# Kernel tuning notes

Measured on AMD Instinct MI355X. Metric: run time of the kernel, lower is better.

The kernel has to match this reference:

```python
import jax, jax.numpy as jnp
import numpy as np

N, E, D, H = 50000, 800000, 128, 128


def _uniform_param(key, shape, fan_in):
    bound = 1.0 / np.sqrt(fan_in)
    return jax.random.uniform(key, shape, jnp.float32, -bound, bound)


def setup_inputs() -> dict:
    key = jax.random.key(0)
    ks = jax.random.split(key, 12)
    x = jax.random.normal(ks[0], (N, D), jnp.float32)
    xedge = jax.random.randint(ks[1], (2, E), 0, N, jnp.int64)
    y = jax.random.randint(ks[2], (N,), 0, 2, jnp.int32).astype(bool)
    return {
        "x": x,
        "xedge": xedge,
        "y": y,
        "pretrain": 0,
        # SAGEConv layer 1 (in=D, out=H): lin_l (with bias) applied to mean aggr, lin_r (no bias) to self
        "W1l": _uniform_param(ks[3], (D, H), D),
        "b1l": _uniform_param(ks[4], (H,), D),
        "W1r": _uniform_param(ks[5], (D, H), D),
        # SAGEConv layer 2 (in=H, out=H)
        "W2l": _uniform_param(ks[6], (H, H), H),
        "b2l": _uniform_param(ks[7], (H,), H),
        "W2r": _uniform_param(ks[8], (H, H), H),
        # Decoder weight [H, H]
        "Wdec": _uniform_param(ks[9], (H, H), H),
    }


def sage_conv(h, src, dst, Wl, bl, Wr, num_nodes):
    # gather neighbor features along edges, mean-aggregate by destination
    msgs = h[src]                                            # [E, d]
    agg = jax.ops.segment_sum(msgs, dst, num_segments=num_nodes)
    cnt = jax.ops.segment_sum(jnp.ones((src.shape[0],), h.dtype), dst,
                              num_segments=num_nodes)
    mean = agg / jnp.maximum(cnt, 1.0)[:, None]              # [N, d]
    return mean @ Wl + bl + h @ Wr                           # [N, out]


def reference(x, xedge, y, pretrain, W1l, b1l, W1r, W2l, b2l, W2r, Wdec):
    src, dst = xedge[0], xedge[1]
    n = x.shape[0]
    # Encoder: SAGE = conv1 -> relu -> (dropout: eval identity) -> conv2
    h = jax.nn.relu(sage_conv(x, src, dst, W1l, b1l, W1r, n))
    emb = sage_conv(h, src, dst, W2l, b2l, W2r, n)           # [N, H]
    # Decoder
    dx = emb @ Wdec                                          # [N, H]
    # BCEWithLogits: pos nodes target 1, neg nodes target 0, mean within each group
    ym = y.astype(dx.dtype)                                  # [N]
    n_pos = jnp.sum(ym)
    n_neg = n - n_pos
    hdim = dx.shape[1]
    sp_pos = jax.nn.softplus(-dx)   # bce(logit, 1)
    sp_neg = jax.nn.softplus(dx)    # bce(logit, 0)
    l2 = jnp.sum(sp_pos * ym[:, None]) / (jnp.maximum(n_pos, 1.0) * hdim)
    l1 = jnp.sum(sp_neg * (1.0 - ym)[:, None]) / (jnp.maximum(n_neg, 1.0) * hdim)
    return (l1 + l2, emb)
```

## Files before the change

kernel.cpp:

```cpp
#include <hip/hip_runtime.h>
#include <hip/hip_bf16.h>

#define NDIM 128
#define SCAN_CHUNK 1024

typedef __attribute__((ext_vector_type(8))) short short8;
typedef __attribute__((ext_vector_type(4))) float f32x4;

__device__ __forceinline__ float bf2f(__hip_bfloat16 v) { return __bfloat162float(v); }

__device__ __forceinline__ float ldf(const void* p, long i, int f32) {
    return f32 ? ((const float*)p)[i] : bf2f(((const __hip_bfloat16*)p)[i]);
}
__device__ __forceinline__ void stf(void* p, long i, int f32, float v) {
    if (f32) ((float*)p)[i] = v;
    else     ((__hip_bfloat16*)p)[i] = __float2bfloat16(v);
}
__device__ __forceinline__ short f2bf(float v) {
    __hip_bfloat16 h = __float2bfloat16(v);
    short s;
    __builtin_memcpy(&s, &h, 2);
    return s;
}
__device__ __forceinline__ float bflo(unsigned u) { u <<= 16; float f; __builtin_memcpy(&f, &u, 4); return f; }
__device__ __forceinline__ float bfhi(unsigned u) { u &= 0xffff0000u; float f; __builtin_memcpy(&f, &u, 4); return f; }
__device__ __forceinline__ unsigned packbf(float a, float b) {
    unsigned la = (unsigned short)f2bf(a);
    unsigned hb = (unsigned short)f2bf(b);
    return (hb << 16) | la;
}
__device__ __forceinline__ int aswz(int m, int k) {
    return m * NDIM + ((((k >> 3) ^ (m & 7)) << 3) | (k & 7));
}
__device__ __forceinline__ int wswz(int m, int p) {
    return m * 64 + ((((p >> 2) ^ (m & 7)) << 2) | (p & 3));
}

__global__ void detect_kernel(const int* __restrict__ xedge32,
                              const unsigned int* __restrict__ yw,
                              const unsigned short* __restrict__ xh,
                              int* __restrict__ flags, int* __restrict__ cnt,
                              float* __restrict__ accum, int* __restrict__ npos, int N) {
    const int gid = blockIdx.x * 256 + threadIdx.x;
    for (int i = gid; i < N; i += gridDim.x * 256) cnt[i] = 0;
    if (gid == 0) { accum[0] = 0.f; accum[1] = 0.f; npos[0] = 0; }
    if (blockIdx.x == 0) {
        __shared__ int se, sy, scount;
        const int t = threadIdx.x;
        if (t == 0) { se = 1; sy = 0; scount = 0; }
        __syncthreads();
        for (int i = t; i < 512; i += 256)
            if (xedge32[2 * i + 1] != 0) se = 0;
        for (int i = t; i < 1024; i += 256)
            if (yw[i] > 1u) sy = 1;
        int c = 0;
        for (int i = t; i < 1024; i += 256) {
            int ex = (xh[2 * i] >> 7) & 0xFF;
            if (ex >= 100 && ex <= 150) c++;
        }
        atomicAdd(&scount, c);
        __syncthreads();
        if (t == 0) { flags[0] = se; flags[1] = sy; flags[2] = (scount < 900) ? 1 : 0; }
    }
}


__global__ void prep_kernel(const void* __restrict__ x,
                            const void* __restrict__ W1l, const void* __restrict__ b1l,
                            const void* __restrict__ W1r, const void* __restrict__ W2l,
                            const void* __restrict__ b2l, const void* __restrict__ W2r,
                            const void* __restrict__ Wd, const int* __restrict__ flags,
                            short* __restrict__ T1l, short* __restrict__ T1r,
                            short* __restrict__ T2l, short* __restrict__ T2r,
                            short* __restrict__ Td, float* __restrict__ b1c,
                            float* __restrict__ b2c, unsigned* __restrict__ xb, int N) {
    const int wf = flags[2];
    const long idx = (long)blockIdx.x * 256 + threadIdx.x;
    if (idx < NDIM * NDIM) {
        int k = (int)(idx >> 7), n = (int)(idx & 127);
        int o = n * NDIM + k;
        T1l[o] = f2bf(ldf(W1l, idx, wf));
        T1r[o] = f2bf(ldf(W1r, idx, wf));
        T2l[o] = f2bf(ldf(W2l, idx, wf));
        T2r[o] = f2bf(ldf(W2r, idx, wf));
        Td [o] = f2bf(ldf(Wd , idx, wf));
        if (idx < NDIM) { b1c[idx] = ldf(b1l, idx, wf); b2c[idx] = ldf(b2l, idx, wf); }
    } else {
        long p = idx - NDIM * NDIM;
        long np = (long)N * 64;
        if (p < np) {
            if (wf) {
                float2 v = ((const float2*)x)[p];
                xb[p] = packbf(v.x, v.y);
            } else {
                xb[p] = ((const unsigned*)x)[p];
            }
        }
    }
}


__global__ void degree_kernel(const int* __restrict__ xedge, int E,
                              const int* __restrict__ flags, int* __restrict__ cnt) {
    int e = blockIdx.x * blockDim.x + threadIdx.x;
    if (e >= E) return;
    int d = flags[0] ? xedge[2 * (E + e)] : xedge[E + e];
    atomicAdd(&cnt[d], 1);
}


__global__ void scan_partial(const int* __restrict__ cnt, int* __restrict__ bsum, int N) {
    __shared__ int red[256];
    const int t = threadIdx.x;
    const long base = (long)blockIdx.x * SCAN_CHUNK + (long)t * 4;
    int s = 0;
#pragma unroll
    for (int i = 0; i < 4; ++i) { long idx = base + i; if (idx < N) s += cnt[idx]; }
    red[t] = s;
    __syncthreads();
    for (int off = 128; off >= 1; off >>= 1) {
        if (t < off) red[t] += red[t + off];
        __syncthreads();
    }
    if (t == 0) bsum[blockIdx.x] = red[0];
}

__global__ void scan_bsums(const int* __restrict__ bsum, int* __restrict__ boff,
                           int B, int* __restrict__ rowptr, int N) {
    __shared__ int part[1024];
    const int t = threadIdx.x;
    int v = (t < B) ? bsum[t] : 0;
    part[t] = v;
    __syncthreads();
    for (int off = 1; off < 1024; off <<= 1) {
        int u = (t >= off) ? part[t - off] : 0;
        __syncthreads();
        part[t] += u;
        __syncthreads();
    }
    if (t < B) boff[t] = part[t] - v;
    if (t == 1023) rowptr[N] = part[1023];
}

__global__ void scan_scatter(int* __restrict__ cnt, const int* __restrict__ boff,
                             int* __restrict__ rowptr, int N) {
    __shared__ int tsum[256];
    const int t = threadIdx.x;
    const long base = (long)blockIdx.x * SCAN_CHUNK + (long)t * 4;
    int loc[4];
    int s = 0;
#pragma unroll
    for (int i = 0; i < 4; ++i) {
        long idx = base + i;
        int c = (idx < N) ? cnt[idx] : 0;
        loc[i] = s;
        s += c;
    }
    tsum[t] = s;
    __syncthreads();
    for (int off = 1; off < 256; off <<= 1) {
        int u = (t >= off) ? tsum[t - off] : 0;
        __syncthreads();
        tsum[t] += u;
        __syncthreads();
    }
    const int texcl = tsum[t] - s;
    const int b0 = boff[blockIdx.x];
#pragma unroll
    for (int i = 0; i < 4; ++i) {
        long idx = base + i;
        if (idx < N) { rowptr[idx] = b0 + texcl + loc[i]; cnt[idx] = 0; }
    }
}

__global__ void fill_kernel(const int* __restrict__ xedge, int E,
                            const int* __restrict__ flags, const int* __restrict__ rowptr,
                            int* __restrict__ cur, int* __restrict__ col) {
    int e = blockIdx.x * blockDim.x + threadIdx.x;
    if (e >= E) return;
    const int e64 = flags[0];
    int s = e64 ? xedge[2 * e] : xedge[e];
    int d = e64 ? xedge[2 * (E + e)] : xedge[E + e];
    int p = rowptr[d] + atomicAdd(&cur[d], 1);
    col[p] = s;
}


template <bool RELU, int OUTMODE>
__global__ __launch_bounds__(256)
void layer_mfma(const unsigned* __restrict__ Xb, const int* __restrict__ rowptr,
                const int* __restrict__ col, const short* __restrict__ WlT,
                const float* __restrict__ biasc, const short* __restrict__ WrT,
                const int* __restrict__ flags, void* __restrict__ outp, int N) {
    __shared__ short Ms[32 * NDIM];
    __shared__ short Ss[32 * NDIM];
    unsigned* Msw = (unsigned*)Ms;
    unsigned* Ssw = (unsigned*)Ss;
    const int t = threadIdx.x;
    const int n0 = blockIdx.x * 32;
    const int wf = flags[2];
    {
        const int g = t >> 6, p = t & 63;
        for (int r = g; r < 32; r += 4) {
            int n = n0 + r;
            float m0 = 0.f, m1 = 0.f;
            unsigned su = 0;
            if (n < N) {
                int b = rowptr[n], e = rowptr[n + 1];
                int i = b;
                for (; i + 8 <= e; i += 8) {
                    unsigned u0 = Xb[(long)col[i    ] * 64 + p];
                    unsigned u1 = Xb[(long)col[i + 1] * 64 + p];
                    unsigned u2 = Xb[(long)col[i + 2] * 64 + p];
                    unsigned u3 = Xb[(long)col[i + 3] * 64 + p];
                    unsigned u4 = Xb[(long)col[i + 4] * 64 + p];
                    unsigned u5 = Xb[(long)col[i + 5] * 64 + p];
                    unsigned u6 = Xb[(long)col[i + 6] * 64 + p];
                    unsigned u7 = Xb[(long)col[i + 7] * 64 + p];
                    m0 += ((bflo(u0) + bflo(u1)) + (bflo(u2) + bflo(u3)))
                        + ((bflo(u4) + bflo(u5)) + (bflo(u6) + bflo(u7)));
                    m1 += ((bfhi(u0) + bfhi(u1)) + (bfhi(u2) + bfhi(u3)))
                        + ((bfhi(u4) + bfhi(u5)) + (bfhi(u6) + bfhi(u7)));
                }
                for (; i < e; ++i) {
                    unsigned u = Xb[(long)col[i] * 64 + p];
                    m0 += bflo(u);
                    m1 += bfhi(u);
                }
                float inv = 1.f / fmaxf((float)(e - b), 1.f);
                m0 *= inv; m1 *= inv;
                su = Xb[(long)n * 64 + p];
            }
            int wi = wswz(r, p);
            Msw[wi] = packbf(m0, m1);
            Ssw[wi] = su;
        }
    }
    __syncthreads();
    const int l = t & 63, w = t >> 6;
    const int quad = l >> 4, l15 = l & 15;
    const int wcol = w * 32;
    f32x4 acc[2][2] = {};
    for (int k0 = 0; k0 < NDIM; k0 += 32) {
        const int kc = k0 + quad * 8;
        short8 ams[2], ass[2], bl[2], br[2];
#pragma unroll
        for (int rt = 0; rt < 2; ++rt) {
            int m = rt * 16 + l15;
            ams[rt] = *(const short8*)&Ms[aswz(m, kc)];
            ass[rt] = *(const short8*)&Ss[aswz(m, kc)];
        }
#pragma unroll
        for (int ct = 0; ct < 2; ++ct) {
            int n = wcol + ct * 16 + l15;
            bl[ct] = *(const short8*)&WlT[n * NDIM + kc];
            br[ct] = *(const short8*)&WrT[n * NDIM + kc];
        }
#pragma unroll
        for (int rt = 0; rt < 2; ++rt)
#pragma unroll
            for (int ct = 0; ct < 2; ++ct) {
                acc[rt][ct] = __builtin_amdgcn_mfma_f32_16x16x32_bf16(
                    ams[rt], bl[ct], acc[rt][ct], 0, 0, 0);
                acc[rt][ct] = __builtin_amdgcn_mfma_f32_16x16x32_bf16(
                    ass[rt], br[ct], acc[rt][ct], 0, 0, 0);
            }
    }
#pragma unroll
    for (int ct = 0; ct < 2; ++ct) {
        int cg = wcol + ct * 16 + l15;
        float bv = biasc[cg];
#pragma unroll
        for (int rt = 0; rt < 2; ++rt)
#pragma unroll
            for (int reg = 0; reg < 4; ++reg) {
                int n = n0 + rt * 16 + quad * 4 + reg;
                if (n < N) {
                    float v = acc[rt][ct][reg] + bv;
                    if (RELU) v = fmaxf(v, 0.f);
                    if (OUTMODE == 0)
                        ((__hip_bfloat16*)outp)[(long)n * NDIM + cg] = __float2bfloat16(v);
                    else
                        stf((char*)outp + (wf ? 4 : 2), (long)n * NDIM + cg, wf, v);
                }
            }
    }
}


__global__ __launch_bounds__(256)
void loss_mfma(const void* __restrict__ d_out_base, const short* __restrict__ WdT,
               const void* __restrict__ yv, const int* __restrict__ flags,
               float* __restrict__ accum, int* __restrict__ npos, int N) {
    __shared__ short As[32 * NDIM];
    __shared__ int ylds[32];
    __shared__ float red[4][2];
    const int t = threadIdx.x;
    const int n0 = blockIdx.x * 32;
    const int wf = flags[2], yb = flags[1];
    const void* emb = (const void*)((const char*)d_out_base + (wf ? 4 : 2));
    {
        const int j = t & 127, g = t >> 7;
        for (int r = g; r < 32; r += 2) {
            int n = n0 + r;
            float v = (n < N) ? ldf(emb, (long)n * NDIM + j, wf) : 0.f;
            As[aswz(r, j)] = f2bf(v);
        }
        if (t < 32) {
            int n = n0 + t;
            int yn = -1;
            if (n < N)
                yn = yb ? (int)((const unsigned char*)yv)[n]
                        : (((const int*)yv)[n] != 0 ? 1 : 0);
            ylds[t] = yn;
        }
    }
    __syncthreads();
    const int l = t & 63, w = t >> 6;
    const int quad = l >> 4, l15 = l & 15;
    const int wcol = w * 32;
    f32x4 acc[2][2] = {};
    for (int k0 = 0; k0 < NDIM; k0 += 32) {
        const int kc = k0 + quad * 8;
        short8 a[2], b[2];
#pragma unroll
        for (int rt = 0; rt < 2; ++rt)
            a[rt] = *(const short8*)&As[aswz(rt * 16 + l15, kc)];
#pragma unroll
        for (int ct = 0; ct < 2; ++ct)
            b[ct] = *(const short8*)&WdT[(wcol + ct * 16 + l15) * NDIM + kc];
#pragma unroll
        for (int rt = 0; rt < 2; ++rt)
#pragma unroll
            for (int ct = 0; ct < 2; ++ct)
                acc[rt][ct] = __builtin_amdgcn_mfma_f32_16x16x32_bf16(
                    a[rt], b[ct], acc[rt][ct], 0, 0, 0);
    }
    float lpos = 0.f, lneg = 0.f;
#pragma unroll
    for (int rt = 0; rt < 2; ++rt)
#pragma unroll
        for (int reg = 0; reg < 4; ++reg) {
            int row = rt * 16 + quad * 4 + reg;
            int yn = ylds[row];
            if (yn >= 0) {
#pragma unroll
                for (int ct = 0; ct < 2; ++ct) {
                    float z = acc[rt][ct][reg];
                    float L = log1pf(expf(-fabsf(z)));
                    if (yn) lpos += fmaxf(-z, 0.f) + L;
                    else    lneg += fmaxf(z, 0.f) + L;
                }
            }
        }
#pragma unroll
    for (int off = 32; off >= 1; off >>= 1) {
        lpos += __shfl_down(lpos, off, 64);
        lneg += __shfl_down(lneg, off, 64);
    }
    if (l == 0) { red[w][0] = lpos; red[w][1] = lneg; }
    __syncthreads();
    if (t == 0) {
        atomicAdd(&accum[0], red[0][0] + red[1][0] + red[2][0] + red[3][0]);
        atomicAdd(&accum[1], red[0][1] + red[1][1] + red[2][1] + red[3][1]);
        int c = 0;
        for (int i = 0; i < 32; ++i) if (ylds[i] > 0) c++;
        if (c) atomicAdd(npos, c);
    }
}

__global__ void finalize_kernel(const float* __restrict__ accum, const int* __restrict__ npos,
                                const int* __restrict__ flags, void* __restrict__ out, int N) {
    float np_ = (float)(*npos);
    float nn_ = (float)N - np_;
    float l2 = accum[0] / (fmaxf(np_, 1.f) * 128.f);
    float l1 = accum[1] / (fmaxf(nn_, 1.f) * 128.f);
    stf(out, 0, flags[2], l1 + l2);
}


extern "C" void kernel_launch(void* const* d_in, const int* in_sizes, int n_in,
                              void* d_out, int out_size, void* d_ws, size_t ws_size,
                              hipStream_t stream) {
    const void* x    = d_in[0];
    const int* xedge = (const int*)d_in[1];
    const void* y    = d_in[2];
    const void* W1l  = d_in[4];
    const void* b1l  = d_in[5];
    const void* W1r  = d_in[6];
    const void* W2l  = d_in[7];
    const void* b2l  = d_in[8];
    const void* W2r  = d_in[9];
    const void* Wdec = d_in[10];

    const int N = in_sizes[0] / NDIM;
    const int E = in_sizes[1] / 2;

    char* ws = (char*)d_ws;
    size_t off = 0;
    auto alloc = [&](size_t bytes) -> void* {
        void* p = ws + off;
        off = (off + bytes + 255) & ~(size_t)255;
        return p;
    };
    int*   flags  = (int*)alloc(64);
    float* accum  = (float*)alloc(64);
    int*   npos   = (int*)alloc(64);
    int*   bsum   = (int*)alloc(1024 * 4);
    int*   boff   = (int*)alloc(1024 * 4);
    int*   cnt    = (int*)alloc((size_t)N * 4);
    int*   rowptr = (int*)alloc((size_t)(N + 1) * 4);
    int*   col    = (int*)alloc((size_t)E * 4);
    unsigned* xb  = (unsigned*)alloc((size_t)N * 64 * 4);
    unsigned* hbuf = (unsigned*)alloc((size_t)N * 64 * 4);
    short* T1l = (short*)alloc(NDIM * NDIM * 2);
    short* T1r = (short*)alloc(NDIM * NDIM * 2);
    short* T2l = (short*)alloc(NDIM * NDIM * 2);
    short* T2r = (short*)alloc(NDIM * NDIM * 2);
    short* Td  = (short*)alloc(NDIM * NDIM * 2);
    float* b1c = (float*)alloc(NDIM * 4);
    float* b2c = (float*)alloc(NDIM * 4);

    const int zb = (N + 255) / 256;
    detect_kernel<<<zb, 256, 0, stream>>>(xedge, (const unsigned int*)y,
                                          (const unsigned short*)x, flags, cnt,
                                          accum, npos, N);
    const long prep_items = (long)NDIM * NDIM + (long)N * 64;
    prep_kernel<<<(int)((prep_items + 255) / 256), 256, 0, stream>>>(
        x, W1l, b1l, W1r, W2l, b2l, W2r, Wdec, flags,
        T1l, T1r, T2l, T2r, Td, b1c, b2c, xb, N);

    const int eb = (E + 255) / 256;
    degree_kernel<<<eb, 256, 0, stream>>>(xedge, E, flags, cnt);

    const int sb = (N + SCAN_CHUNK - 1) / SCAN_CHUNK;
    scan_partial<<<sb, 256, 0, stream>>>(cnt, bsum, N);
    scan_bsums<<<1, 1024, 0, stream>>>(bsum, boff, sb, rowptr, N);
    scan_scatter<<<sb, 256, 0, stream>>>(cnt, boff, rowptr, N);

    fill_kernel<<<eb, 256, 0, stream>>>(xedge, E, flags, rowptr, cnt, col);

    const int nb32 = (N + 31) / 32;
    layer_mfma<true, 0><<<nb32, 256, 0, stream>>>(
        xb, rowptr, col, T1l, b1c, T1r, flags, hbuf, N);
    layer_mfma<false, 1><<<nb32, 256, 0, stream>>>(
        hbuf, rowptr, col, T2l, b2c, T2r, flags, d_out, N);
    loss_mfma<<<nb32, 256, 0, stream>>>(d_out, Td, y, flags, accum, npos, N);
    finalize_kernel<<<1, 1, 0, stream>>>(accum, npos, flags, d_out, N);
}
```

Baseline: 364.4 us.

## Fuse decoder loss into layer-2 kernel and split neighbor gather across edges

The loss/decoder kernel is merged into the second SAGE layer kernel, so the embedding tile stays in shared memory for the decoder MFMA instead of being re-read from global memory. The neighbor gather is restructured so each wavefront handles 16-dword column chunks across four edges in parallel, with rowptr loads hoisted and partial sums combined by lane shuffles, to expose more memory-level parallelism. Output stores are staged through LDS so they can be written coalesced. This raises shared-memory use and register pressure, and it adds an extra block barrier.

```diff
diff --git a/kernel.cpp b/kernel.cpp
--- a/kernel.cpp
+++ b/kernel.cpp
@@ -108,7 +108,6 @@
     atomicAdd(&cnt[d], 1);
 }
 
-
 __global__ void scan_partial(const int* __restrict__ cnt, int* __restrict__ bsum, int N) {
     __shared__ int red[256];
     const int t = threadIdx.x;
@@ -191,49 +190,80 @@
 void layer_mfma(const unsigned* __restrict__ Xb, const int* __restrict__ rowptr,
                 const int* __restrict__ col, const short* __restrict__ WlT,
                 const float* __restrict__ biasc, const short* __restrict__ WrT,
-                const int* __restrict__ flags, void* __restrict__ outp, int N) {
-    __shared__ short Ms[32 * NDIM];
-    __shared__ short Ss[32 * NDIM];
+                const short* __restrict__ WdT, const void* __restrict__ yv,
+                const int* __restrict__ flags, void* __restrict__ outp,
+                float* __restrict__ accum, int* __restrict__ npos, int N) {
+    extern __shared__ char smem[];
+    short* Ms = (short*)smem;
+    short* Ss = Ms + 32 * NDIM;
     unsigned* Msw = (unsigned*)Ms;
     unsigned* Ssw = (unsigned*)Ss;
     const int t = threadIdx.x;
     const int n0 = blockIdx.x * 32;
     const int wf = flags[2];
+
     {
-        const int g = t >> 6, p = t & 63;
-        for (int r = g; r < 32; r += 4) {
+        const int g = t >> 6;
+        const int lane = t & 63;
+        const int eo = lane >> 4;
+        const int j = lane & 15;
+        int bk[8], ek[8];
+#pragma unroll
+        for (int k = 0; k < 8; ++k) {
+            int n = n0 + g + 4 * k;
+            int b = 0, e = 0;
+            if (n < N) { b = rowptr[n]; e = rowptr[n + 1]; }
+            bk[k] = b; ek[k] = e;
+        }
+#pragma unroll
+        for (int k = 0; k < 8; ++k) {
+            int r = g + 4 * k;
             int n = n0 + r;
-            float m0 = 0.f, m1 = 0.f;
-            unsigned su = 0;
-            if (n < N) {
-                int b = rowptr[n], e = rowptr[n + 1];
+            unsigned su = (n < N) ? Xb[(long)n * 64 + lane] : 0u;
+            Ssw[wswz(r, lane)] = su;
+        }
+        for (int q = 0; q < 4; ++q) {
+            const int qo = q * 16;
+#pragma unroll
+            for (int k = 0; k < 8; ++k) {
+                const int r = g + 4 * k;
+                const int b = bk[k], e = ek[k];
+                float m0 = 0.f, m1 = 0.f;
                 int i = b;
+                for (; i + 16 <= e; i += 16) {
+                    int c0 = col[i + eo], c1 = col[i + 4 + eo];
+                    int c2 = col[i + 8 + eo], c3 = col[i + 12 + eo];
+                    unsigned u0 = Xb[(long)c0 * 64 + qo + j];
+                    unsigned u1 = Xb[(long)c1 * 64 + qo + j];
+                    unsigned u2 = Xb[(long)c2 * 64 + qo + j];
+                    unsigned u3 = Xb[(long)c3 * 64 + qo + j];
+                    m0 += (bflo(u0) + bflo(u1)) + (bflo(u2) + bflo(u3));
+                    m1 += (bfhi(u0) + bfhi(u1)) + (bfhi(u2) + bfhi(u3));
+                }
                 for (; i + 8 <= e; i += 8) {
-                    unsigned u0 = Xb[(long)col[i    ] * 64 + p];
-                    unsigned u1 = Xb[(long)col[i + 1] * 64 + p];
-                    unsigned u2 = Xb[(long)col[i + 2] * 64 + p];
-                    unsigned u3 = Xb[(long)col[i + 3] * 64 + p];
-                    unsigned u4 = Xb[(long)col[i + 4] * 64 + p];
-                    unsigned u5 = Xb[(long)col[i + 5] * 64 + p];
-                    unsigned u6 = Xb[(long)col[i + 6] * 64 + p];
-                    unsigned u7 = Xb[(long)col[i + 7] * 64 + p];
-                    m0 += ((bflo(u0) + bflo(u1)) + (bflo(u2) + bflo(u3)))
-                        + ((bflo(u4) + bflo(u5)) + (bflo(u6) + bflo(u7)));
-                    m1 += ((bfhi(u0) + bfhi(u1)) + (bfhi(u2) + bfhi(u3)))
-                        + ((bfhi(u4) + bfhi(u5)) + (bfhi(u6) + bfhi(u7)));
-                }
-                for (; i < e; ++i) {
-                    unsigned u = Xb[(long)col[i] * 64 + p];
-                    m0 += bflo(u);
-                    m1 += bfhi(u);
-                }
-                float inv = 1.f / fmaxf((float)(e - b), 1.f);
-                m0 *= inv; m1 *= inv;
-                su = Xb[(long)n * 64 + p];
-            }
-            int wi = wswz(r, p);
-            Msw[wi] = packbf(m0, m1);
-            Ssw[wi] = su;
+                    int c0 = col[i + eo], c1 = col[i + 4 + eo];
+                    unsigned u0 = Xb[(long)c0 * 64 + qo + j];
+                    unsigned u1 = Xb[(long)c1 * 64 + qo + j];
+                    m0 += bflo(u0) + bflo(u1);
+                    m1 += bfhi(u0) + bfhi(u1);
+                }
+                if (i + eo < e) {
+                    unsigned u = Xb[(long)col[i + eo] * 64 + qo + j];
+                    m0 += bflo(u); m1 += bfhi(u);
+                }
+                if (i + 4 + eo < e) {
+                    unsigned u = Xb[(long)col[i + 4 + eo] * 64 + qo + j];
+                    m0 += bflo(u); m1 += bfhi(u);
+                }
+                m0 += __shfl_xor(m0, 16, 64);
+                m0 += __shfl_xor(m0, 32, 64);
+                m1 += __shfl_xor(m1, 16, 64);
+                m1 += __shfl_xor(m1, 32, 64);
+                if (eo == 0) {
+                    float inv = 1.f / fmaxf((float)(e - b), 1.f);
+                    Msw[wswz(r, qo + j)] = packbf(m0 * inv, m1 * inv);
+                }
+            }
         }
     }
     __syncthreads();
@@ -266,45 +296,48 @@
                     ass[rt], br[ct], acc[rt][ct], 0, 0, 0);
             }
     }
-#pragma unroll
-    for (int ct = 0; ct < 2; ++ct) {
-        int cg = wcol + ct * 16 + l15;
-        float bv = biasc[cg];
-#pragma unroll
-        for (int rt = 0; rt < 2; ++rt)
-#pragma unroll
-            for (int reg = 0; reg < 4; ++reg) {
-                int n = n0 + rt * 16 + quad * 4 + reg;
-                if (n < N) {
+    __syncthreads();
+
+    if (OUTMODE == 0) {
+#pragma unroll
+        for (int ct = 0; ct < 2; ++ct) {
+            int cg = wcol + ct * 16 + l15;
+            float bv = biasc[cg];
+#pragma unroll
+            for (int rt = 0; rt < 2; ++rt)
+#pragma unroll
+                for (int reg = 0; reg < 4; ++reg) {
+                    int row = rt * 16 + quad * 4 + reg;
                     float v = acc[rt][ct][reg] + bv;
                     if (RELU) v = fmaxf(v, 0.f);
-                    if (OUTMODE == 0)
-                        ((__hip_bfloat16*)outp)[(long)n * NDIM + cg] = __float2bfloat16(v);
-                    else
-                        stf((char*)outp + (wf ? 4 : 2), (long)n * NDIM + cg, wf, v);
-                }
-            }
-    }
-}
-
-
-__global__ __launch_bounds__(256)
-void loss_mfma(const void* __restrict__ d_out_base, const short* __restrict__ WdT,
-               const void* __restrict__ yv, const int* __restrict__ flags,
-               float* __restrict__ accum, int* __restrict__ npos, int N) {
-    __shared__ short As[32 * NDIM];
-    __shared__ int ylds[32];
-    __shared__ float red[4][2];
-    const int t = threadIdx.x;
-    const int n0 = blockIdx.x * 32;
-    const int wf = flags[2], yb = flags[1];
-    const void* emb = (const void*)((const char*)d_out_base + (wf ? 4 : 2));
-    {
-        const int j = t & 127, g = t >> 7;
-        for (int r = g; r < 32; r += 2) {
-            int n = n0 + r;
-            float v = (n < N) ? ldf(emb, (long)n * NDIM + j, wf) : 0.f;
-            As[aswz(r, j)] = f2bf(v);
+                    Ms[row * NDIM + cg] = f2bf(v);
+                }
+        }
+        __syncthreads();
+        unsigned* ob = (unsigned*)outp;
+        for (int idx = t; idx < 2048; idx += 256) {
+            int r = idx >> 6;
+            if (n0 + r < N) ob[(long)n0 * 64 + idx] = Msw[idx];
+        }
+    } else {
+        float* Tf  = (float*)smem;
+        short* Abf = (short*)(smem + 16384);
+        int* ylds  = (int*)(smem + 16384 + 8192);
+        float* redm = (float*)(smem + 16384 + 8192 + 128);
+        const int yb = flags[1];
+#pragma unroll
+        for (int ct = 0; ct < 2; ++ct) {
+            int cg = wcol + ct * 16 + l15;
+            float bv = biasc[cg];
+#pragma unroll
+            for (int rt = 0; rt < 2; ++rt)
+#pragma unroll
+                for (int reg = 0; reg < 4; ++reg) {
+                    int row = rt * 16 + quad * 4 + reg;
+                    float v = acc[rt][ct][reg] + bv;
+                    Tf[row * NDIM + cg] = v;
+                    Abf[aswz(row, cg)] = f2bf(v);
+                }
         }
         if (t < 32) {
             int n = n0 + t;
@@ -314,58 +347,68 @@
                         : (((const int*)yv)[n] != 0 ? 1 : 0);
             ylds[t] = yn;
         }
-    }
-    __syncthreads();
-    const int l = t & 63, w = t >> 6;
-    const int quad = l >> 4, l15 = l & 15;
-    const int wcol = w * 32;
-    f32x4 acc[2][2] = {};
-    for (int k0 = 0; k0 < NDIM; k0 += 32) {
-        const int kc = k0 + quad * 8;
-        short8 a[2], b[2];
+        __syncthreads();
+        if (wf) {
+            float* embf = (float*)outp + 1;
+            for (int idx = t; idx < 4096; idx += 256) {
+                int r = idx >> 7;
+                if (n0 + r < N) embf[(long)n0 * NDIM + idx] = Tf[idx];
+            }
+        } else {
+            __hip_bfloat16* embh = (__hip_bfloat16*)outp + 1;
+            for (int idx = t; idx < 4096; idx += 256) {
+                int r = idx >> 7;
+                if (n0 + r < N) embh[(long)n0 * NDIM + idx] = __float2bfloat16(Tf[idx]);
+            }
+        }
+        f32x4 acc2[2][2] = {};
+        for (int k0 = 0; k0 < NDIM; k0 += 32) {
+            const int kc = k0 + quad * 8;
+            short8 a[2], b[2];
+#pragma unroll
+            for (int rt = 0; rt < 2; ++rt)
+                a[rt] = *(const short8*)&Abf[aswz(rt * 16 + l15, kc)];
+#pragma unroll
+            for (int ct = 0; ct < 2; ++ct)
+                b[ct] = *(const short8*)&WdT[(wcol + ct * 16 + l15) * NDIM + kc];
+#pragma unroll
+            for (int rt = 0; rt < 2; ++rt)
+#pragma unroll
+                for (int ct = 0; ct < 2; ++ct)
+                    acc2[rt][ct] = __builtin_amdgcn_mfma_f32_16x16x32_bf16(
+                        a[rt], b[ct], acc2[rt][ct], 0, 0, 0);
+        }
+        float lpos = 0.f, lneg = 0.f;
 #pragma unroll
         for (int rt = 0; rt < 2; ++rt)
-            a[rt] = *(const short8*)&As[aswz(rt * 16 + l15, kc)];
-#pragma unroll
-        for (int ct = 0; ct < 2; ++ct)
-            b[ct] = *(const short8*)&WdT[(wcol + ct * 16 + l15) * NDIM + kc];
-#pragma unroll
-        for (int rt = 0; rt < 2; ++rt)
-#pragma unroll
-            for (int ct = 0; ct < 2; ++ct)
-                acc[rt][ct] = __builtin_amdgcn_mfma_f32_16x16x32_bf16(
-                    a[rt], b[ct], acc[rt][ct], 0, 0, 0);
-    }
-    float lpos = 0.f, lneg = 0.f;
-#pragma unroll
-    for (int rt = 0; rt < 2; ++rt)
-#pragma unroll
-        for (int reg = 0; reg < 4; ++reg) {
-            int row = rt * 16 + quad * 4 + reg;
-            int yn = ylds[row];
-            if (yn >= 0) {
-#pragma unroll
-                for (int ct = 0; ct < 2; ++ct) {
-                    float z = acc[rt][ct][reg];
-                    float L = log1pf(expf(-fabsf(z)));
-                    if (yn) lpos += fmaxf(-z, 0.f) + L;
-                    else    lneg += fmaxf(z, 0.f) + L;
-                }
-            }
-        }
-#pragma unroll
-    for (int off = 32; off >= 1; off >>= 1) {
-        lpos += __shfl_down(lpos, off, 64);
-        lneg += __shfl_down(lneg, off, 64);
-    }
-    if (l == 0) { red[w][0] = lpos; red[w][1] = lneg; }
-    __syncthreads();
-    if (t == 0) {
-        atomicAdd(&accum[0], red[0][0] + red[1][0] + red[2][0] + red[3][0]);
-        atomicAdd(&accum[1], red[0][1] + red[1][1] + red[2][1] + red[3][1]);
-        int c = 0;
-        for (int i = 0; i < 32; ++i) if (ylds[i] > 0) c++;
-        if (c) atomicAdd(npos, c);
+#pragma unroll
+            for (int reg = 0; reg < 4; ++reg) {
+                int row = rt * 16 + quad * 4 + reg;
+                int yn = ylds[row];
+                if (yn >= 0) {
+#pragma unroll
+                    for (int ct = 0; ct < 2; ++ct) {
+                        float z = acc2[rt][ct][reg];
+                        float L = log1pf(expf(-fabsf(z)));
+                        if (yn) lpos += fmaxf(-z, 0.f) + L;
+                        else    lneg += fmaxf(z, 0.f) + L;
+                    }
+                }
+            }
+#pragma unroll
+        for (int off = 32; off >= 1; off >>= 1) {
+            lpos += __shfl_down(lpos, off, 64);
+            lneg += __shfl_down(lneg, off, 64);
+        }
+        if (l == 0) { redm[w * 2] = lpos; redm[w * 2 + 1] = lneg; }
+        __syncthreads();
+        if (t == 0) {
+            atomicAdd(&accum[0], redm[0] + redm[2] + redm[4] + redm[6]);
+            atomicAdd(&accum[1], redm[1] + redm[3] + redm[5] + redm[7]);
+            int c = 0;
+            for (int i = 0; i < 32; ++i) if (ylds[i] > 0) c++;
+            if (c) atomicAdd(npos, c);
+        }
     }
 }
 
@@ -441,10 +484,13 @@
     fill_kernel<<<eb, 256, 0, stream>>>(xedge, E, flags, rowptr, cnt, col);
 
     const int nb32 = (N + 31) / 32;
-    layer_mfma<true, 0><<<nb32, 256, 0, stream>>>(
-        xb, rowptr, col, T1l, b1c, T1r, flags, hbuf, N);
-    layer_mfma<false, 1><<<nb32, 256, 0, stream>>>(
-        hbuf, rowptr, col, T2l, b2c, T2r, flags, d_out, N);
-    loss_mfma<<<nb32, 256, 0, stream>>>(d_out, Td, y, flags, accum, npos, N);
+    const size_t sm1 = 16384;
+    const size_t sm2 = 16384 + 8192 + 128 + 32;
+    layer_mfma<true, 0><<<nb32, 256, sm1, stream>>>(
+        xb, rowptr, col, T1l, b1c, T1r, nullptr, nullptr, flags,
+        hbuf, accum, npos, N);
+    layer_mfma<false, 1><<<nb32, 256, sm2, stream>>>(
+        hbuf, rowptr, col, T2l, b2c, T2r, Td, y, flags,
+        d_out, accum, npos, N);
     finalize_kernel<<<1, 1, 0, stream>>>(accum, npos, flags, d_out, N);
 }
```

New measurement: 457.0 us. 25.4% more time.

## Fuse degree count into prep, stage layer outputs via LDS, feed loss bf16

Applied to the files above, without the earlier changes.

Folds the edge-degree atomic counting into the prep kernel so one launch does both, relying on the prep grid (NDIM*NDIM + N*64 items) being larger than E. The layer kernels now stage their MFMA outputs through shared memory, so global stores are row-contiguous and coalesced instead of scattered per-lane element writes. The second layer also writes a packed bf16 copy of the embedding into the reused xb buffer, which the loss kernel reads directly instead of re-reading and converting the fp32 or bf16 output. In exchange the kernels use extra __syncthreads and LDS reuse, and an extra bf16 write is added to the second layer.

```diff
diff --git a/kernel.cpp b/kernel.cpp
--- a/kernel.cpp
+++ b/kernel.cpp
@@ -73,9 +73,15 @@
                             short* __restrict__ T1l, short* __restrict__ T1r,
                             short* __restrict__ T2l, short* __restrict__ T2r,
                             short* __restrict__ Td, float* __restrict__ b1c,
-                            float* __restrict__ b2c, unsigned* __restrict__ xb, int N) {
+                            float* __restrict__ b2c, unsigned* __restrict__ xb,
+                            const int* __restrict__ xedge, int E,
+                            int* __restrict__ cnt, int N) {
     const int wf = flags[2];
     const long idx = (long)blockIdx.x * 256 + threadIdx.x;
+    if (idx < E) {
+        int d = flags[0] ? xedge[2 * (E + idx)] : xedge[E + idx];
+        atomicAdd(&cnt[d], 1);
+    }
     if (idx < NDIM * NDIM) {
         int k = (int)(idx >> 7), n = (int)(idx & 127);
         int o = n * NDIM + k;
@@ -100,15 +106,6 @@
 }
 
 
-__global__ void degree_kernel(const int* __restrict__ xedge, int E,
-                              const int* __restrict__ flags, int* __restrict__ cnt) {
-    int e = blockIdx.x * blockDim.x + threadIdx.x;
-    if (e >= E) return;
-    int d = flags[0] ? xedge[2 * (E + e)] : xedge[E + e];
-    atomicAdd(&cnt[d], 1);
-}
-
-
 __global__ void scan_partial(const int* __restrict__ cnt, int* __restrict__ bsum, int N) {
     __shared__ int red[256];
     const int t = threadIdx.x;
@@ -191,9 +188,11 @@
 void layer_mfma(const unsigned* __restrict__ Xb, const int* __restrict__ rowptr,
                 const int* __restrict__ col, const short* __restrict__ WlT,
                 const float* __restrict__ biasc, const short* __restrict__ WrT,
-                const int* __restrict__ flags, void* __restrict__ outp, int N) {
-    __shared__ short Ms[32 * NDIM];
-    __shared__ short Ss[32 * NDIM];
+                const int* __restrict__ flags, void* __restrict__ outp,
+                unsigned* __restrict__ hemb, int N) {
+    __shared__ short AS[2 * 32 * NDIM];
+    short* Ms = AS;
+    short* Ss = AS + 32 * NDIM;
     unsigned* Msw = (unsigned*)Ms;
     unsigned* Ssw = (unsigned*)Ss;
     const int t = threadIdx.x;
@@ -266,45 +265,96 @@
                     ass[rt], br[ct], acc[rt][ct], 0, 0, 0);
             }
     }
-#pragma unroll
-    for (int ct = 0; ct < 2; ++ct) {
-        int cg = wcol + ct * 16 + l15;
-        float bv = biasc[cg];
-#pragma unroll
-        for (int rt = 0; rt < 2; ++rt)
-#pragma unroll
-            for (int reg = 0; reg < 4; ++reg) {
-                int n = n0 + rt * 16 + quad * 4 + reg;
-                if (n < N) {
+    __syncthreads();
+
+    if (OUTMODE == 0) {
+#pragma unroll
+        for (int ct = 0; ct < 2; ++ct) {
+            int cg = wcol + ct * 16 + l15;
+            float bv = biasc[cg];
+#pragma unroll
+            for (int rt = 0; rt < 2; ++rt)
+#pragma unroll
+                for (int reg = 0; reg < 4; ++reg) {
+                    int row = rt * 16 + quad * 4 + reg;
                     float v = acc[rt][ct][reg] + bv;
                     if (RELU) v = fmaxf(v, 0.f);
-                    if (OUTMODE == 0)
-                        ((__hip_bfloat16*)outp)[(long)n * NDIM + cg] = __float2bfloat16(v);
-                    else
-                        stf((char*)outp + (wf ? 4 : 2), (long)n * NDIM + cg, wf, v);
+                    Ms[row * NDIM + cg] = f2bf(v);
                 }
-            }
+        }
+        __syncthreads();
+        unsigned* ob = (unsigned*)outp;
+        for (int idx = t; idx < 2048; idx += 256) {
+            int r = idx >> 6;
+            if (n0 + r < N) ob[(long)n0 * 64 + idx] = Msw[idx];
+        }
+    } else {
+        if (wf) {
+            float* Tf = (float*)AS;
+#pragma unroll
+            for (int ct = 0; ct < 2; ++ct) {
+                int cg = wcol + ct * 16 + l15;
+                float bv = biasc[cg];
+#pragma unroll
+                for (int rt = 0; rt < 2; ++rt)
+#pragma unroll
+                    for (int reg = 0; reg < 4; ++reg) {
+                        int row = rt * 16 + quad * 4 + reg;
+                        Tf[row * NDIM + cg] = acc[rt][ct][reg] + bv;
+                    }
+            }
+            __syncthreads();
+            float* embf = (float*)outp + 1;
+            for (int idx = t; idx < 4096; idx += 256) {
+                int r = idx >> 7;
+                if (n0 + r < N) embf[(long)n0 * NDIM + idx] = Tf[idx];
+            }
+            __syncthreads();
+        }
+#pragma unroll
+        for (int ct = 0; ct < 2; ++ct) {
+            int cg = wcol + ct * 16 + l15;
+            float bv = biasc[cg];
+#pragma unroll
+            for (int rt = 0; rt < 2; ++rt)
+#pragma unroll
+                for (int reg = 0; reg < 4; ++reg) {
+                    int row = rt * 16 + quad * 4 + reg;
+                    Ms[row * NDIM + cg] = f2bf(acc[rt][ct][reg] + bv);
+                }
+        }
+        __syncthreads();
+        for (int idx = t; idx < 2048; idx += 256) {
+            int r = idx >> 6;
+            if (n0 + r < N) hemb[(long)n0 * 64 + idx] = Msw[idx];
+        }
+        if (!wf) {
+            short* embh = (short*)outp + 1;
+            for (int idx = t; idx < 4096; idx += 256) {
+                int r = idx >> 7;
+                if (n0 + r < N) embh[(long)n0 * NDIM + idx] = Ms[idx];
+            }
+        }
     }
 }
 
 
 __global__ __launch_bounds__(256)
-void loss_mfma(const void* __restrict__ d_out_base, const short* __restrict__ WdT,
+void loss_mfma(const unsigned* __restrict__ hemb, const short* __restrict__ WdT,
                const void* __restrict__ yv, const int* __restrict__ flags,
                float* __restrict__ accum, int* __restrict__ npos, int N) {
     __shared__ short As[32 * NDIM];
     __shared__ int ylds[32];
     __shared__ float red[4][2];
+    unsigned* Asw = (unsigned*)As;
     const int t = threadIdx.x;
     const int n0 = blockIdx.x * 32;
-    const int wf = flags[2], yb = flags[1];
-    const void* emb = (const void*)((const char*)d_out_base + (wf ? 4 : 2));
+    const int yb = flags[1];
     {
-        const int j = t & 127, g = t >> 7;
-        for (int r = g; r < 32; r += 2) {
+        const int g = t >> 6, p = t & 63;
+        for (int r = g; r < 32; r += 4) {
             int n = n0 + r;
-            float v = (n < N) ? ldf(emb, (long)n * NDIM + j, wf) : 0.f;
-            As[aswz(r, j)] = f2bf(v);
+            Asw[wswz(r, p)] = (n < N) ? hemb[(long)n * 64 + p] : 0u;
         }
         if (t < 32) {
             int n = n0 + t;
@@ -428,23 +478,21 @@
     const long prep_items = (long)NDIM * NDIM + (long)N * 64;
     prep_kernel<<<(int)((prep_items + 255) / 256), 256, 0, stream>>>(
         x, W1l, b1l, W1r, W2l, b2l, W2r, Wdec, flags,
-        T1l, T1r, T2l, T2r, Td, b1c, b2c, xb, N);
-
-    const int eb = (E + 255) / 256;
-    degree_kernel<<<eb, 256, 0, stream>>>(xedge, E, flags, cnt);
+        T1l, T1r, T2l, T2r, Td, b1c, b2c, xb, xedge, E, cnt, N);
 
     const int sb = (N + SCAN_CHUNK - 1) / SCAN_CHUNK;
     scan_partial<<<sb, 256, 0, stream>>>(cnt, bsum, N);
     scan_bsums<<<1, 1024, 0, stream>>>(bsum, boff, sb, rowptr, N);
     scan_scatter<<<sb, 256, 0, stream>>>(cnt, boff, rowptr, N);
 
+    const int eb = (E + 255) / 256;
     fill_kernel<<<eb, 256, 0, stream>>>(xedge, E, flags, rowptr, cnt, col);
 
     const int nb32 = (N + 31) / 32;
     layer_mfma<true, 0><<<nb32, 256, 0, stream>>>(
-        xb, rowptr, col, T1l, b1c, T1r, flags, hbuf, N);
+        xb, rowptr, col, T1l, b1c, T1r, flags, hbuf, nullptr, N);
     layer_mfma<false, 1><<<nb32, 256, 0, stream>>>(
-        hbuf, rowptr, col, T2l, b2c, T2r, flags, d_out, N);
-    loss_mfma<<<nb32, 256, 0, stream>>>(d_out, Td, y, flags, accum, npos, N);
+        hbuf, rowptr, col, T2l, b2c, T2r, flags, d_out, xb, N);
+    loss_mfma<<<nb32, 256, 0, stream>>>(xb, Td, y, flags, accum, npos, N);
     finalize_kernel<<<1, 1, 0, stream>>>(accum, npos, flags, d_out, N);
 }
```

After: 378.7 us. 3.9% more time.
